# Kernel tuning notes

Measured on AMD Instinct MI355X. Metric: run time of the kernel, lower is better.

Reference implementation:

```python
import jax, jax.numpy as jnp
import numpy as np

N_NODES = 200000
IN_DIM = 128
HID = 64
WALK_LEN = 16          # max_step + 1
NUM_WALKS = 16         # = hidden_graphs, walks per graph
N_GRAPHS = 1024
PEN = 32
N_CLASSES = 10
BN_EPS = 1e-5


def setup_inputs() -> dict:
    key = jax.random.key(0)
    ks = jax.random.split(key, 16)
    x = jax.random.normal(ks[0], (N_NODES, IN_DIM), dtype=jnp.float32)
    walks = jax.random.randint(ks[1], (N_GRAPHS * NUM_WALKS, WALK_LEN), 0, N_NODES)
    # each graph contributes NUM_WALKS consecutive walks
    walk_batch = jnp.repeat(jnp.arange(N_GRAPHS), NUM_WALKS)
    s = 1.0 / np.sqrt(HID)
    return {
        "x": x,
        "walks": walks,
        "walk_batch": walk_batch,
        "W_enc": jax.random.normal(ks[2], (HID, IN_DIM), jnp.float32) / np.sqrt(IN_DIM),
        "b_enc": jnp.zeros((HID,), jnp.float32),
        "W_ih": jax.random.uniform(ks[3], (3 * HID, HID), jnp.float32, -s, s),
        "W_hh": jax.random.uniform(ks[4], (3 * HID, HID), jnp.float32, -s, s),
        "b_ih": jax.random.uniform(ks[5], (3 * HID,), jnp.float32, -s, s),
        "b_hh": jax.random.uniform(ks[6], (3 * HID,), jnp.float32, -s, s),
        "gamma": jnp.ones((HID,), jnp.float32),
        "beta": jnp.zeros((HID,), jnp.float32),
        "W1": jax.random.normal(ks[7], (PEN, HID), jnp.float32) / np.sqrt(HID),
        "b1": jnp.zeros((PEN,), jnp.float32),
        "W2": jax.random.normal(ks[8], (N_CLASSES, PEN), jnp.float32) / np.sqrt(PEN),
        "b2": jnp.zeros((N_CLASSES,), jnp.float32),
    }


def _gru_cell(h, xt, W_ih, W_hh, b_ih, b_hh):
    # PyTorch GRU gate math
    gi = xt @ W_ih.T + b_ih            # [W, 3H]
    gh = h @ W_hh.T + b_hh             # [W, 3H]
    i_r, i_z, i_n = jnp.split(gi, 3, axis=-1)
    h_r, h_z, h_n = jnp.split(gh, 3, axis=-1)
    r = jax.nn.sigmoid(i_r + h_r)
    z = jax.nn.sigmoid(i_z + h_z)
    n = jnp.tanh(i_n + r * h_n)
    return (1.0 - z) * n + z * h


def reference(x, walks, walk_batch, W_enc, b_enc, W_ih, W_hh, b_ih, b_hh,
              gamma, beta, W1, b1, W2, b2):
    # feature encoder on all nodes, then gather along walks
    x_enc = x @ W_enc.T + b_enc                     # [N, H]
    walk_feats = x_enc[walks]                       # [W, L, H] gather
    xs = jnp.swapaxes(walk_feats, 0, 1)             # [L, W, H]

    def step(h, xt):
        return _gru_cell(h, xt, W_ih, W_hh, b_ih, b_hh), None

    h0 = jnp.zeros((walks.shape[0], HID), walk_feats.dtype)
    h_final, _ = jax.lax.scan(step, h0, xs)         # [W, H] last hidden state

    # segment-mean pooling per graph
    seg_sum = jax.ops.segment_sum(h_final, walk_batch, num_segments=N_GRAPHS)
    cnt = jax.ops.segment_sum(jnp.ones((walks.shape[0],), h_final.dtype),
                              walk_batch, num_segments=N_GRAPHS)
    graph_enc = seg_sum / jnp.maximum(cnt, 1.0)[:, None]   # [B, H]

    # BatchNorm1d (training mode: batch statistics, biased variance)
    mean = jnp.mean(graph_enc, axis=0)
    var = jnp.mean(jnp.square(graph_enc - mean), axis=0)
    gn = (graph_enc - mean) / jnp.sqrt(var + BN_EPS) * gamma + beta

    h1 = jax.nn.relu(gn @ W1.T + b1)                # dropout p=0 -> identity
    logits = h1 @ W2.T + b2
    return jax.nn.log_softmax(logits, axis=1)
```

## Files before the change

kernel.cpp:

```cpp
#include <hip/hip_runtime.h>
#include <stdint.h>

typedef _Float16 half8 __attribute__((ext_vector_type(8)));
typedef _Float16 half4 __attribute__((ext_vector_type(4)));
typedef float f32x4 __attribute__((ext_vector_type(4)));

#define MFMA_F16(A, B, C) __builtin_amdgcn_mfma_f32_16x16x32_f16(A, B, C, 0, 0, 0)

#define NN 200000
#define NT 3125
#define GSTRIDE 512

__device__ __forceinline__ void gload_lds16(const void* gp, void* lp) {
  __builtin_amdgcn_global_load_lds(
      (const __attribute__((address_space(1))) uint32_t*)(gp),
      (__attribute__((address_space(3))) uint32_t*)(lp), 16, 0, 0);
}

__global__ __launch_bounds__(256, 2) void k_enc(const float* __restrict__ x,
                                                const float* __restrict__ Wenc,
                                                const float* __restrict__ benc,
                                                _Float16* __restrict__ xenc) {
  __shared__ float xl[2][64 * 128];
  __shared__ _Float16 wlds[16 * 64 * 8];

  const int tid = threadIdx.x;
  const int lane = tid & 63, wv = tid >> 6;
  const int r = lane & 15, g = lane >> 4;

  const int t0 = blockIdx.x;
#pragma unroll
  for (int i = 0; i < 8; ++i) {
    int row = wv * 16 + 2 * i + (lane >> 5);
    int grow = t0 * 64 + row;
    if (grow >= NN) grow = NN - 1;
    int scol = ((lane & 31) * 16) ^ ((row & 7) << 4);
    gload_lds16((const char*)(x + (size_t)grow * 128) + scol,
                (char*)&xl[0][0] + (wv * 16 + 2 * i) * 512);
  }

  for (int i4 = tid; i4 < 2048; i4 += 256) {
    int idx = i4 * 4;
    f32x4 v = *(const f32x4*)(Wenc + idx);
    int j = idx >> 7, k = idx & 127;
    int tile = (j >> 4) * 4 + (k >> 5);
    int ln = ((k >> 3) & 3) * 16 + (j & 15);
    half4 h;
    h[0] = (_Float16)v[0]; h[1] = (_Float16)v[1];
    h[2] = (_Float16)v[2]; h[3] = (_Float16)v[3];
    *(half4*)&wlds[(tile * 64 + ln) * 8 + (k & 7)] = h;
  }
  __syncthreads();

  half8 W[4][4];
#pragma unroll
  for (int jt = 0; jt < 4; ++jt)
#pragma unroll
    for (int kt = 0; kt < 4; ++kt)
      W[jt][kt] = *(const half8*)&wlds[((jt * 4 + kt) * 64 + lane) * 8];

  float bb[4][4];
#pragma unroll
  for (int jt = 0; jt < 4; ++jt)
#pragma unroll
    for (int rr = 0; rr < 4; ++rr) bb[jt][rr] = benc[jt * 16 + g * 4 + rr];

  const int sw = (r & 7) << 4;
  int buf = 0;

  for (int t = t0; t < NT; t += GSTRIDE) {
    int tn = t + GSTRIDE;
    if (tn < NT) {
#pragma unroll
      for (int i = 0; i < 8; ++i) {
        int row = wv * 16 + 2 * i + (lane >> 5);
        int grow = tn * 64 + row;
        if (grow >= NN) grow = NN - 1;
        int scol = ((lane & 31) * 16) ^ ((row & 7) << 4);
        gload_lds16((const char*)(x + (size_t)grow * 128) + scol,
                    (char*)&xl[buf ^ 1][0] + (wv * 16 + 2 * i) * 512);
      }
      asm volatile("s_waitcnt vmcnt(8)" ::: "memory");
    } else {
      asm volatile("s_waitcnt vmcnt(0)" ::: "memory");
    }
    __builtin_amdgcn_sched_barrier(0);

    const char* rp = (const char*)&xl[buf][0] + (wv * 16 + r) * 512;
    f32x4 acc[4];
#pragma unroll
    for (int jt = 0; jt < 4; ++jt)
      acc[jt] = (f32x4){bb[jt][0], bb[jt][1], bb[jt][2], bb[jt][3]};

#pragma unroll
    for (int kt = 0; kt < 4; ++kt) {
      f32x4 v0 = *(const f32x4*)(rp + ((kt * 128 + g * 32) ^ sw));
      f32x4 v1 = *(const f32x4*)(rp + ((kt * 128 + g * 32 + 16) ^ sw));
      half8 a;
#pragma unroll
      for (int e = 0; e < 4; ++e) {
        a[e] = (_Float16)v0[e];
        a[4 + e] = (_Float16)v1[e];
      }
#pragma unroll
      for (int jt = 0; jt < 4; ++jt)
        acc[jt] = MFMA_F16(W[jt][kt], a, acc[jt]);
    }

    int node = t * 64 + wv * 16 + r;
    if (node < NN) {
#pragma unroll
      for (int jt = 0; jt < 4; ++jt) {
        half4 o;
        o[0] = (_Float16)acc[jt][0]; o[1] = (_Float16)acc[jt][1];
        o[2] = (_Float16)acc[jt][2]; o[3] = (_Float16)acc[jt][3];
        *(half4*)&xenc[(size_t)node * 64 + jt * 16 + g * 4] = o;
      }
    }
    buf ^= 1;
  }
}

__global__ __launch_bounds__(512, 4) void k_gru(const _Float16* __restrict__ xenc,
                                                const int* __restrict__ walks,
                                                const float* __restrict__ Wih,
                                                const float* __restrict__ Whh,
                                                const float* __restrict__ bih,
                                                const float* __restrict__ bhh,
                                                float* __restrict__ genc) {
  __shared__ _Float16 wih_lds[24 * 64 * 8];
  __shared__ _Float16 whh_lds[24 * 64 * 8];
  __shared__ _Float16 h_lds[2][2][16 * 64];
  __shared__ int ids[2][256];

  const int tid = threadIdx.x;
  const int lane = tid & 63, wv = tid >> 6;
  const int r = lane & 15, g = lane >> 4;
  const int p = wv & 3;
  const int gl = wv >> 2;
  const int gph = blockIdx.x * 2 + gl;

  for (int idx = tid; idx < 192 * 64; idx += 512) {
    int j = idx >> 6, k = idx & 63;
    int tile = (j >> 4) * 2 + (k >> 5);
    int ln = ((k >> 3) & 3) * 16 + (j & 15);
    int off = (tile * 64 + ln) * 8 + (k & 7);
    wih_lds[off] = (_Float16)Wih[idx];
    whh_lds[off] = (_Float16)Whh[idx];
  }

  if ((wv & 3) == 0) {
    const int* wp = walks + gph * 256;
    int4 v = *(const int4*)(wp + lane * 4);
    int vals[4] = {v.x, v.y, v.z, v.w};
#pragma unroll
    for (int i = 0; i < 4; ++i) {
      int m = lane * 4 + i;
      ids[gl][(m & 15) * 16 + (m >> 4)] = vals[i];
    }
  }

  for (int i = tid; i < 4096; i += 512) ((_Float16*)h_lds)[i] = (_Float16)0.f;

  __syncthreads();

  half8 Bi[3][2], Bh[3][2];
#pragma unroll
  for (int G = 0; G < 3; ++G)
#pragma unroll
    for (int kt = 0; kt < 2; ++kt) {
      int T = G * 4 + p;
      Bi[G][kt] = *(const half8*)&wih_lds[((T * 2 + kt) * 64 + lane) * 8];
      Bh[G][kt] = *(const half8*)&whh_lds[((T * 2 + kt) * 64 + lane) * 8];
    }

  const int j0 = p * 16 + r;
  const float br_ = bih[j0] + bhh[j0];
  const float bz_ = bih[64 + j0] + bhh[64 + j0];
  const float bin_ = bih[128 + j0];
  const float bhn_ = bhh[128 + j0];

  f32x4 h = (f32x4){0.f, 0.f, 0.f, 0.f};
  const int swz = (r & 7) << 4;

  half8 AxA0, AxA1, AxB0, AxB1;
  {
    int n0 = ids[gl][0 * 16 + r];
    const _Float16* p0 = xenc + (size_t)n0 * 64 + g * 8;
    AxA0 = *(const half8*)p0;
    AxA1 = *(const half8*)(p0 + 32);
    int n1 = ids[gl][1 * 16 + r];
    const _Float16* p1 = xenc + (size_t)n1 * 64 + g * 8;
    AxB0 = *(const half8*)p1;
    AxB1 = *(const half8*)(p1 + 32);
  }

#define GRU_STEP(T_, RB, AX0, AX1)                                             \
  {                                                                            \
              \
    int nid = ids[gl][(((T_) + 2) & 15) * 16 + r];                             \
    const _Float16* xp = xenc + (size_t)nid * 64 + g * 8;                      \
    half8 NX0 = *(const half8*)xp;                                             \
    half8 NX1 = *(const half8*)(xp + 32);                                      \
    char* rbase = (char*)&h_lds[gl][RB][0];                                    \
    char* wbase = (char*)&h_lds[gl][RB ^ 1][0];                                \
    half8 Ah0 = *(const half8*)(rbase + ((r * 128 + g * 16) ^ swz));           \
    half8 Ah1 = *(const half8*)(rbase + ((r * 128 + 64 + g * 16) ^ swz));      \
    f32x4 aR = (f32x4){br_, br_, br_, br_};                                    \
    f32x4 aZ = (f32x4){bz_, bz_, bz_, bz_};                                    \
    f32x4 aN = (f32x4){bin_, bin_, bin_, bin_};                                \
    f32x4 aH = (f32x4){bhn_, bhn_, bhn_, bhn_};                                \
    aR = MFMA_F16(AX0, Bi[0][0], aR);                                          \
    aR = MFMA_F16(AX1, Bi[0][1], aR);                                          \
    aZ = MFMA_F16(AX0, Bi[1][0], aZ);                                          \
    aZ = MFMA_F16(AX1, Bi[1][1], aZ);                                          \
    aN = MFMA_F16(AX0, Bi[2][0], aN);                                          \
    aN = MFMA_F16(AX1, Bi[2][1], aN);                                          \
    aR = MFMA_F16(Ah0, Bh[0][0], aR);                                          \
    aR = MFMA_F16(Ah1, Bh[0][1], aR);                                          \
    aZ = MFMA_F16(Ah0, Bh[1][0], aZ);                                          \
    aZ = MFMA_F16(Ah1, Bh[1][1], aZ);                                          \
    aH = MFMA_F16(Ah0, Bh[2][0], aH);                                          \
    aH = MFMA_F16(Ah1, Bh[2][1], aH);                                          \
    _Pragma("unroll") for (int rr = 0; rr < 4; ++rr) {                         \
      float rg = __builtin_amdgcn_rcpf(1.f + __expf(-aR[rr]));                 \
      float zg = __builtin_amdgcn_rcpf(1.f + __expf(-aZ[rr]));                 \
      float pn = aN[rr] + rg * aH[rr];                                         \
      float e2 = __expf(2.f * pn);                                             \
      float nn = 1.f - 2.f * __builtin_amdgcn_rcpf(e2 + 1.f);                  \
      h[rr] = (1.f - zg) * nn + zg * h[rr];                                    \
    }                                                                          \
    if ((T_) < 15) {                                                           \
      _Pragma("unroll") for (int rr = 0; rr < 4; ++rr) {                       \
        int row = g * 4 + rr;                                                  \
        int byte = (row * 128 + j0 * 2) ^ ((row & 7) << 4);                    \
        *(_Float16*)(wbase + byte) = (_Float16)h[rr];                          \
      }                                                                        \
    }                                                                          \
    asm volatile("s_waitcnt lgkmcnt(0)" ::: "memory");                         \
    __builtin_amdgcn_s_barrier();                                              \
    __builtin_amdgcn_sched_barrier(0);                                         \
    AX0 = NX0;                                                                 \
    AX1 = NX1;                                                                 \
  }

  for (int t = 0; t < 16; t += 2) {
    GRU_STEP(t, 0, AxA0, AxA1);
    GRU_STEP(t + 1, 1, AxB0, AxB1);
  }
#undef GRU_STEP

  {
    float s = h[0] + h[1] + h[2] + h[3];
    s += __shfl_xor(s, 16);
    s += __shfl_xor(s, 32);
    if (g == 0) genc[gph * 64 + j0] = s * 0.0625f;
  }
}

__global__ __launch_bounds__(1024) void k_stats(const float* __restrict__ genc,
                                                const float* __restrict__ gamma,
                                                const float* __restrict__ beta,
                                                float* __restrict__ ss) {
  __shared__ float sum_s[16][64], sq_s[16][64];
  int j = threadIdx.x & 63, grp = threadIdx.x >> 6;
  float s = 0.f, q = 0.f;
#pragma unroll 4
  for (int rr = 0; rr < 64; ++rr) {
    float v = genc[(grp * 64 + rr) * 64 + j];
    s += v;
    q += v * v;
  }
  sum_s[grp][j] = s;
  sq_s[grp][j] = q;
  __syncthreads();
  if (grp == 0) {
    float S = 0.f, Q = 0.f;
#pragma unroll
    for (int k = 0; k < 16; ++k) {
      S += sum_s[k][j];
      Q += sq_s[k][j];
    }
    float mean = S * (1.f / 1024.f);
    float var = Q * (1.f / 1024.f) - mean * mean;
    float rstd = rsqrtf(var + 1e-5f);
    float sc = gamma[j] * rstd;
    ss[j] = sc;
    ss[64 + j] = beta[j] - mean * sc;
  }
}

__global__ __launch_bounds__(256, 1) void k_mlp(const float* __restrict__ genc,
                                                const float* __restrict__ ss,
                                                const float* __restrict__ W1,
                                                const float* __restrict__ b1,
                                                const float* __restrict__ W2,
                                                const float* __restrict__ b2,
                                                float* __restrict__ out) {
  __shared__ float w1[32 * 64], w2[10 * 32], bb1[32], bb2[10], sc[64], sh[64];
  const int tid = threadIdx.x;
  for (int i = tid; i < 32 * 64; i += 256) w1[i] = W1[i];
  for (int i = tid; i < 10 * 32; i += 256) w2[i] = W2[i];
  if (tid < 32) bb1[tid] = b1[tid];
  if (tid >= 32 && tid < 42) bb2[tid - 32] = b2[tid - 32];
  if (tid >= 64 && tid < 128) sc[tid - 64] = ss[tid - 64];
  if (tid >= 128 && tid < 192) sh[tid - 128] = ss[64 + tid - 128];
  __syncthreads();

  const int row = blockIdx.x * 256 + tid;
  float gn[64];
  const f32x4* gp = (const f32x4*)(genc + row * 64);
#pragma unroll
  for (int jq = 0; jq < 16; ++jq) {
    f32x4 v = gp[jq];
#pragma unroll
    for (int e = 0; e < 4; ++e) gn[jq * 4 + e] = v[e] * sc[jq * 4 + e] + sh[jq * 4 + e];
  }

  float h1[32];
#pragma unroll
  for (int i = 0; i < 32; ++i) {
    float a = bb1[i];
#pragma unroll
    for (int j = 0; j < 64; ++j) a += w1[i * 64 + j] * gn[j];
    h1[i] = fmaxf(a, 0.f);
  }

  float lg[10];
  float mx = -1e30f;
#pragma unroll
  for (int c = 0; c < 10; ++c) {
    float a = bb2[c];
#pragma unroll
    for (int i = 0; i < 32; ++i) a += w2[c * 32 + i] * h1[i];
    lg[c] = a;
    mx = fmaxf(mx, a);
  }
  float se = 0.f;
#pragma unroll
  for (int c = 0; c < 10; ++c) se += __expf(lg[c] - mx);
  float lse = mx + __logf(se);
#pragma unroll
  for (int c = 0; c < 10; ++c) out[row * 10 + c] = lg[c] - lse;
}

extern "C" void kernel_launch(void* const* d_in, const int* in_sizes, int n_in,
                              void* d_out, int out_size, void* d_ws, size_t ws_size,
                              hipStream_t stream) {
  const float* x = (const float*)d_in[0];
  const int* walks = (const int*)d_in[1];
  const float* Wenc = (const float*)d_in[3];
  const float* benc = (const float*)d_in[4];
  const float* Wih = (const float*)d_in[5];
  const float* Whh = (const float*)d_in[6];
  const float* bih = (const float*)d_in[7];
  const float* bhh = (const float*)d_in[8];
  const float* gamma = (const float*)d_in[9];
  const float* beta = (const float*)d_in[10];
  const float* W1 = (const float*)d_in[11];
  const float* b1 = (const float*)d_in[12];
  const float* W2 = (const float*)d_in[13];
  const float* b2 = (const float*)d_in[14];
  float* out = (float*)d_out;

  char* ws = (char*)d_ws;
  _Float16* xenc = (_Float16*)ws;
  float* genc = (float*)(ws + 25600000);
  float* ss = (float*)(ws + 25600000 + 262144);

  k_enc<<<dim3(GSTRIDE), dim3(256), 0, stream>>>(x, Wenc, benc, xenc);
  k_gru<<<dim3(512), dim3(512), 0, stream>>>(xenc, walks, Wih, Whh, bih, bhh, genc);
  k_stats<<<dim3(1), dim3(1024), 0, stream>>>(genc, gamma, beta, ss);
  k_mlp<<<dim3(4), dim3(256), 0, stream>>>(genc, ss, W1, b1, W2, b2, out);
}
```

Measured before the change: 82.19 us.

## Replace async LDS loads with register prefetch, split GRU blocks, fuse stats into MLP

The encoder drops the double-buffered global_load_lds path. It now prefetches the next tile into registers and writes it into a single LDS buffer after compute, which halves encoder LDS use. The GRU kernel goes to one graph per 256-thread block and loads its weight fragments straight from global memory into registers, skipping the LDS staging. The BatchNorm stats and MLP kernels are merged into one kernel that each of the 4 blocks recomputes redundantly, saving a launch. One risk is that the register prefetch into a single buffer needs a barrier between the reads of xl and the next writes, and none appears, so there may be a race.

```diff
diff --git a/kernel.cpp b/kernel.cpp
--- a/kernel.cpp
+++ b/kernel.cpp
@@ -11,32 +11,34 @@
 #define NT 3125
 #define GSTRIDE 512
 
-__device__ __forceinline__ void gload_lds16(const void* gp, void* lp) {
-  __builtin_amdgcn_global_load_lds(
-      (const __attribute__((address_space(1))) uint32_t*)(gp),
-      (__attribute__((address_space(3))) uint32_t*)(lp), 16, 0, 0);
+__device__ __forceinline__ half8 cvt8(const float* p) {
+  half8 a;
+#pragma unroll
+  for (int e = 0; e < 8; ++e) a[e] = (_Float16)p[e];
+  return a;
 }
 
 __global__ __launch_bounds__(256, 2) void k_enc(const float* __restrict__ x,
                                                 const float* __restrict__ Wenc,
                                                 const float* __restrict__ benc,
                                                 _Float16* __restrict__ xenc) {
-  __shared__ float xl[2][64 * 128];
+  __shared__ float xl[64 * 128];
   __shared__ _Float16 wlds[16 * 64 * 8];
 
   const int tid = threadIdx.x;
   const int lane = tid & 63, wv = tid >> 6;
   const int r = lane & 15, g = lane >> 4;
+  const int lrh = lane >> 5;
+  const int cg = lane & 31;
 
   const int t0 = blockIdx.x;
+
+  f32x4 xin[8];
 #pragma unroll
   for (int i = 0; i < 8; ++i) {
-    int row = wv * 16 + 2 * i + (lane >> 5);
-    int grow = t0 * 64 + row;
+    int grow = t0 * 64 + wv * 16 + 2 * i + lrh;
     if (grow >= NN) grow = NN - 1;
-    int scol = ((lane & 31) * 16) ^ ((row & 7) << 4);
-    gload_lds16((const char*)(x + (size_t)grow * 128) + scol,
-                (char*)&xl[0][0] + (wv * 16 + 2 * i) * 512);
+    xin[i] = *(const f32x4*)((const char*)(x + (size_t)grow * 128) + cg * 16);
   }
 
   for (int i4 = tid; i4 < 2048; i4 += 256) {
@@ -50,6 +52,12 @@
     h[2] = (_Float16)v[2]; h[3] = (_Float16)v[3];
     *(half4*)&wlds[(tile * 64 + ln) * 8 + (k & 7)] = h;
   }
+
+#pragma unroll
+  for (int i = 0; i < 8; ++i) {
+    int row = wv * 16 + 2 * i + lrh;
+    *(f32x4*)((char*)xl + row * 512 + ((cg * 16) ^ ((row & 7) << 4))) = xin[i];
+  }
   __syncthreads();
 
   half8 W[4][4];
@@ -66,27 +74,19 @@
     for (int rr = 0; rr < 4; ++rr) bb[jt][rr] = benc[jt * 16 + g * 4 + rr];
 
   const int sw = (r & 7) << 4;
-  int buf = 0;
 
   for (int t = t0; t < NT; t += GSTRIDE) {
     int tn = t + GSTRIDE;
     if (tn < NT) {
 #pragma unroll
       for (int i = 0; i < 8; ++i) {
-        int row = wv * 16 + 2 * i + (lane >> 5);
-        int grow = tn * 64 + row;
+        int grow = tn * 64 + wv * 16 + 2 * i + lrh;
         if (grow >= NN) grow = NN - 1;
-        int scol = ((lane & 31) * 16) ^ ((row & 7) << 4);
-        gload_lds16((const char*)(x + (size_t)grow * 128) + scol,
-                    (char*)&xl[buf ^ 1][0] + (wv * 16 + 2 * i) * 512);
+        xin[i] = *(const f32x4*)((const char*)(x + (size_t)grow * 128) + cg * 16);
       }
-      asm volatile("s_waitcnt vmcnt(8)" ::: "memory");
-    } else {
-      asm volatile("s_waitcnt vmcnt(0)" ::: "memory");
-    }
-    __builtin_amdgcn_sched_barrier(0);
-
-    const char* rp = (const char*)&xl[buf][0] + (wv * 16 + r) * 512;
+    }
+
+    const char* rp = (const char*)xl + (wv * 16 + r) * 512;
     f32x4 acc[4];
 #pragma unroll
     for (int jt = 0; jt < 4; ++jt)
@@ -117,62 +117,56 @@
         *(half4*)&xenc[(size_t)node * 64 + jt * 16 + g * 4] = o;
       }
     }
-    buf ^= 1;
-  }
-}
-
-__global__ __launch_bounds__(512, 4) void k_gru(const _Float16* __restrict__ xenc,
+
+    if (tn < NT) {
+#pragma unroll
+      for (int i = 0; i < 8; ++i) {
+        int row = wv * 16 + 2 * i + lrh;
+        *(f32x4*)((char*)xl + row * 512 + ((cg * 16) ^ ((row & 7) << 4))) = xin[i];
+      }
+    }
+  }
+}
+
+__global__ __launch_bounds__(256, 4) void k_gru(const _Float16* __restrict__ xenc,
                                                 const int* __restrict__ walks,
                                                 const float* __restrict__ Wih,
                                                 const float* __restrict__ Whh,
                                                 const float* __restrict__ bih,
                                                 const float* __restrict__ bhh,
                                                 float* __restrict__ genc) {
-  __shared__ _Float16 wih_lds[24 * 64 * 8];
-  __shared__ _Float16 whh_lds[24 * 64 * 8];
-  __shared__ _Float16 h_lds[2][2][16 * 64];
-  __shared__ int ids[2][256];
+  __shared__ _Float16 h_lds[2][16 * 64];
+  __shared__ int ids[256];
 
   const int tid = threadIdx.x;
   const int lane = tid & 63, wv = tid >> 6;
   const int r = lane & 15, g = lane >> 4;
-  const int p = wv & 3;
-  const int gl = wv >> 2;
-  const int gph = blockIdx.x * 2 + gl;
-
-  for (int idx = tid; idx < 192 * 64; idx += 512) {
-    int j = idx >> 6, k = idx & 63;
-    int tile = (j >> 4) * 2 + (k >> 5);
-    int ln = ((k >> 3) & 3) * 16 + (j & 15);
-    int off = (tile * 64 + ln) * 8 + (k & 7);
-    wih_lds[off] = (_Float16)Wih[idx];
-    whh_lds[off] = (_Float16)Whh[idx];
-  }
-
-  if ((wv & 3) == 0) {
+  const int p = wv;
+  const int gph = blockIdx.x;
+
+  half8 Bi[3][2], Bh[3][2];
+#pragma unroll
+  for (int G = 0; G < 3; ++G)
+#pragma unroll
+    for (int kt = 0; kt < 2; ++kt) {
+      int T = G * 4 + p;
+      Bi[G][kt] = cvt8(Wih + (T * 16 + r) * 64 + kt * 32 + g * 8);
+      Bh[G][kt] = cvt8(Whh + (T * 16 + r) * 64 + kt * 32 + g * 8);
+    }
+
+  if (wv == 0) {
     const int* wp = walks + gph * 256;
     int4 v = *(const int4*)(wp + lane * 4);
     int vals[4] = {v.x, v.y, v.z, v.w};
 #pragma unroll
     for (int i = 0; i < 4; ++i) {
       int m = lane * 4 + i;
-      ids[gl][(m & 15) * 16 + (m >> 4)] = vals[i];
-    }
-  }
-
-  for (int i = tid; i < 4096; i += 512) ((_Float16*)h_lds)[i] = (_Float16)0.f;
+      ids[(m & 15) * 16 + (m >> 4)] = vals[i];
+    }
+  }
+  for (int i = tid; i < 2048; i += 256) ((_Float16*)h_lds)[i] = (_Float16)0.f;
 
   __syncthreads();
-
-  half8 Bi[3][2], Bh[3][2];
-#pragma unroll
-  for (int G = 0; G < 3; ++G)
-#pragma unroll
-    for (int kt = 0; kt < 2; ++kt) {
-      int T = G * 4 + p;
-      Bi[G][kt] = *(const half8*)&wih_lds[((T * 2 + kt) * 64 + lane) * 8];
-      Bh[G][kt] = *(const half8*)&whh_lds[((T * 2 + kt) * 64 + lane) * 8];
-    }
 
   const int j0 = p * 16 + r;
   const float br_ = bih[j0] + bhh[j0];
@@ -185,11 +179,11 @@
 
   half8 AxA0, AxA1, AxB0, AxB1;
   {
-    int n0 = ids[gl][0 * 16 + r];
+    int n0 = ids[0 * 16 + r];
     const _Float16* p0 = xenc + (size_t)n0 * 64 + g * 8;
     AxA0 = *(const half8*)p0;
     AxA1 = *(const half8*)(p0 + 32);
-    int n1 = ids[gl][1 * 16 + r];
+    int n1 = ids[1 * 16 + r];
     const _Float16* p1 = xenc + (size_t)n1 * 64 + g * 8;
     AxB0 = *(const half8*)p1;
     AxB1 = *(const half8*)(p1 + 32);
@@ -197,13 +191,12 @@
 
 #define GRU_STEP(T_, RB, AX0, AX1)                                             \
   {                                                                            \
-              \
-    int nid = ids[gl][(((T_) + 2) & 15) * 16 + r];                             \
+    int nid = ids[(((T_) + 2) & 15) * 16 + r];                                 \
     const _Float16* xp = xenc + (size_t)nid * 64 + g * 8;                      \
     half8 NX0 = *(const half8*)xp;                                             \
     half8 NX1 = *(const half8*)(xp + 32);                                      \
-    char* rbase = (char*)&h_lds[gl][RB][0];                                    \
-    char* wbase = (char*)&h_lds[gl][RB ^ 1][0];                                \
+    char* rbase = (char*)&h_lds[RB][0];                                        \
+    char* wbase = (char*)&h_lds[RB ^ 1][0];                                    \
     half8 Ah0 = *(const half8*)(rbase + ((r * 128 + g * 16) ^ swz));           \
     half8 Ah1 = *(const half8*)(rbase + ((r * 128 + 64 + g * 16) ^ swz));      \
     f32x4 aR = (f32x4){br_, br_, br_, br_};                                    \
@@ -258,53 +251,44 @@
   }
 }
 
-__global__ __launch_bounds__(1024) void k_stats(const float* __restrict__ genc,
-                                                const float* __restrict__ gamma,
-                                                const float* __restrict__ beta,
-                                                float* __restrict__ ss) {
-  __shared__ float sum_s[16][64], sq_s[16][64];
-  int j = threadIdx.x & 63, grp = threadIdx.x >> 6;
+__global__ __launch_bounds__(256) void k_post(const float* __restrict__ genc,
+                                              const float* __restrict__ gamma,
+                                              const float* __restrict__ beta,
+                                              const float* __restrict__ W1,
+                                              const float* __restrict__ b1,
+                                              const float* __restrict__ W2,
+                                              const float* __restrict__ b2,
+                                              float* __restrict__ out) {
+  __shared__ float sum_s[4][64], sq_s[4][64], sc[64], sh[64];
+  __shared__ float w1[32 * 64], w2[10 * 32], bb1[32], bb2[10];
+  const int tid = threadIdx.x;
+  const int j = tid & 63, grp = tid >> 6;
+
   float s = 0.f, q = 0.f;
-#pragma unroll 4
-  for (int rr = 0; rr < 64; ++rr) {
-    float v = genc[(grp * 64 + rr) * 64 + j];
+  for (int rr = 0; rr < 256; ++rr) {
+    float v = genc[(grp * 256 + rr) * 64 + j];
     s += v;
     q += v * v;
   }
   sum_s[grp][j] = s;
   sq_s[grp][j] = q;
-  __syncthreads();
-  if (grp == 0) {
-    float S = 0.f, Q = 0.f;
-#pragma unroll
-    for (int k = 0; k < 16; ++k) {
-      S += sum_s[k][j];
-      Q += sq_s[k][j];
-    }
-    float mean = S * (1.f / 1024.f);
-    float var = Q * (1.f / 1024.f) - mean * mean;
-    float rstd = rsqrtf(var + 1e-5f);
-    float sc = gamma[j] * rstd;
-    ss[j] = sc;
-    ss[64 + j] = beta[j] - mean * sc;
-  }
-}
-
-__global__ __launch_bounds__(256, 1) void k_mlp(const float* __restrict__ genc,
-                                                const float* __restrict__ ss,
-                                                const float* __restrict__ W1,
-                                                const float* __restrict__ b1,
-                                                const float* __restrict__ W2,
-                                                const float* __restrict__ b2,
-                                                float* __restrict__ out) {
-  __shared__ float w1[32 * 64], w2[10 * 32], bb1[32], bb2[10], sc[64], sh[64];
-  const int tid = threadIdx.x;
+
   for (int i = tid; i < 32 * 64; i += 256) w1[i] = W1[i];
   for (int i = tid; i < 10 * 32; i += 256) w2[i] = W2[i];
   if (tid < 32) bb1[tid] = b1[tid];
   if (tid >= 32 && tid < 42) bb2[tid - 32] = b2[tid - 32];
-  if (tid >= 64 && tid < 128) sc[tid - 64] = ss[tid - 64];
-  if (tid >= 128 && tid < 192) sh[tid - 128] = ss[64 + tid - 128];
+  __syncthreads();
+
+  if (grp == 0) {
+    float S = sum_s[0][j] + sum_s[1][j] + sum_s[2][j] + sum_s[3][j];
+    float Q = sq_s[0][j] + sq_s[1][j] + sq_s[2][j] + sq_s[3][j];
+    float mean = S * (1.f / 1024.f);
+    float var = Q * (1.f / 1024.f) - mean * mean;
+    float rstd = rsqrtf(var + 1e-5f);
+    float scv = gamma[j] * rstd;
+    sc[j] = scv;
+    sh[j] = beta[j] - mean * scv;
+  }
   __syncthreads();
 
   const int row = blockIdx.x * 256 + tid;
@@ -322,7 +306,7 @@
   for (int i = 0; i < 32; ++i) {
     float a = bb1[i];
 #pragma unroll
-    for (int j = 0; j < 64; ++j) a += w1[i * 64 + j] * gn[j];
+    for (int jj = 0; jj < 64; ++jj) a += w1[i * 64 + jj] * gn[jj];
     h1[i] = fmaxf(a, 0.f);
   }
 
@@ -366,10 +350,8 @@
   char* ws = (char*)d_ws;
   _Float16* xenc = (_Float16*)ws;
   float* genc = (float*)(ws + 25600000);
-  float* ss = (float*)(ws + 25600000 + 262144);
 
   k_enc<<<dim3(GSTRIDE), dim3(256), 0, stream>>>(x, Wenc, benc, xenc);
-  k_gru<<<dim3(512), dim3(512), 0, stream>>>(xenc, walks, Wih, Whh, bih, bhh, genc);
-  k_stats<<<dim3(1), dim3(1024), 0, stream>>>(genc, gamma, beta, ss);
-  k_mlp<<<dim3(4), dim3(256), 0, stream>>>(genc, ss, W1, b1, W2, b2, out);
-}
+  k_gru<<<dim3(1024), dim3(256), 0, stream>>>(xenc, walks, Wih, Whh, bih, bhh, genc);
+  k_post<<<dim3(4), dim3(256), 0, stream>>>(genc, gamma, beta, W1, b1, W2, b2, out);
+}
```

Result: slower. 88.20 us (+7.3%).
